# Performance work log

Hardware: AMD Instinct MI355X
Metric: run time of the kernel (lower is better)

## Reference

```python
import jax, jax.numpy as jnp
import numpy as np
from jax import lax

B, C_IN, C_OUT, K, STYLE_DIM, H, W = 8, 512, 512, 3, 512, 64, 64


def setup_inputs() -> dict:
    key = jax.random.key(0)
    k1, k2, k3, k4 = jax.random.split(key, 4)
    return {
        "x": jax.random.normal(k1, (B, C_IN, H, W), dtype=jnp.float32),
        "style": jax.random.normal(k2, (B, STYLE_DIM), dtype=jnp.float32),
        "w": jax.random.normal(k3, (1, C_OUT, C_IN, K, K), dtype=jnp.float32),
        "affine_w": jax.random.normal(k4, (C_IN, STYLE_DIM), dtype=jnp.float32),
        "affine_b": jnp.ones((C_IN,), dtype=jnp.float32),  # bias_init=1
    }


def _per_sample_conv(xi, wi):
    # xi: [C_in, H, W], wi: [C_out, C_in, K, K]; 'same' padding, stride 1
    p = K // 2
    out = lax.conv_general_dilated(
        xi[None], wi, window_strides=(1, 1), padding=[(p, p), (p, p)],
        dimension_numbers=("NCHW", "OIHW", "NCHW"))
    return out[0]


def reference(x, style, w, affine_w, affine_b):
    # Affine (FullyConnected_Layer, linear act, lr_multiplier=1)
    weight_gain_fc = 1.0 / np.sqrt(STYLE_DIM)
    s = style @ (affine_w * weight_gain_fc).T + affine_b  # [B, C_in]

    # Modulate
    weight_gain = 1.0 / np.sqrt(C_IN * K * K)
    weight = w * weight_gain * s[:, None, :, None, None]  # [B, C_out, C_in, K, K]

    # Demodulate
    decoefs = lax.rsqrt(jnp.sum(weight * weight, axis=(2, 3, 4)) + 1e-8)  # [B, C_out]
    weight = weight * decoefs[:, :, None, None, None]

    # Per-sample conv (equivalent to groups=B grouped conv2d)
    out = jax.vmap(_per_sample_conv)(x, weight)  # [B, C_out, H, W]
    return out
```

## Files before the change

kernel.cpp:

```cpp
#include <hip/hip_runtime.h>
#include <hip/hip_bf16.h>


#define CDIM 512
#define HW 64
#define CK 32
#define NCHUNK 16

typedef __attribute__((ext_vector_type(8))) short short8;
typedef __attribute__((ext_vector_type(4))) float float4v;

__device__ __forceinline__ short f2bf(float f) {
    unsigned u = __float_as_uint(f);
    unsigned r = (u + 0x7FFFu + ((u >> 16) & 1u)) >> 16;
    return (short)r;
}

__device__ __forceinline__ void async_ld16(const short* g, short* l) {
    __builtin_amdgcn_global_load_lds(
        (const __attribute__((address_space(1))) void*)g,
        (__attribute__((address_space(3))) void*)l, 16, 0, 0);
}

__device__ __forceinline__ void hard_sync() {
    asm volatile("s_waitcnt vmcnt(0) lgkmcnt(0)" ::: "memory");
    __builtin_amdgcn_sched_barrier(0);
    __builtin_amdgcn_s_barrier();
    __builtin_amdgcn_sched_barrier(0);
}


__global__ void k_affine(const float* __restrict__ style, const float* __restrict__ aw,
                         const float* __restrict__ ab, float* __restrict__ s) {
    int b = blockIdx.x;
    int ci = blockIdx.y * 256 + threadIdx.x;
    const float* st = style + b * CDIM;
    const float* w = aw + ci * CDIM;
    float acc = 0.f;
    for (int k = 0; k < CDIM; ++k) acc += st[k] * w[k];
    s[b * CDIM + ci] = acc * 0.04419417382415922f + ab[ci];
}

__global__ void k_ws2(const float* __restrict__ w, float* __restrict__ ws2) {
    int i = blockIdx.x * 256 + threadIdx.x;
    const float* p = w + i * 9;
    float a = 0.f;
#pragma unroll
    for (int t = 0; t < 9; ++t) a += p[t] * p[t];
    ws2[i] = a;
}

__global__ void k_oscale(const float* __restrict__ s, const float* __restrict__ ws2,
                         float* __restrict__ osc) {
    __shared__ float s2[CDIM];
    int b = blockIdx.x;
    int co = blockIdx.y * 256 + threadIdx.x;
    for (int i = threadIdx.x; i < CDIM; i += 256) {
        float v = s[b * CDIM + i];
        s2[i] = v * v;
    }
    __syncthreads();
    const float* r = ws2 + co * CDIM;
    float acc = 0.f;
    for (int k = 0; k < CDIM; ++k) acc += s2[k] * r[k];
    const float wg = 0.014731391274719739f;
    const float wg2 = 2.170138888888889e-4f;
    osc[b * CDIM + co] = wg * rsqrtf(wg2 * acc + 1e-8f);
}

__global__ void k_wconv(const float* __restrict__ w, short* __restrict__ wgt) {
    int idx = blockIdx.x * 256 + threadIdx.x;
    int j = idx & 7;
    int slotg = idx >> 3;
    int region = slotg / 4608;
    int a16 = slotg - region * 4608;
    int tm = a16 >> 6;
    int t = tm >> 3;
    int mf = tm & 7;
    int sl = a16 & 63;
    int l4 = sl >> 4;
    int l15 = sl & 15;
    int ct = region & 3;
    int c = region >> 2;
    int co = ct * 128 + mf * 16 + l15;
    int ci = c * 32 + l4 * 8 + j;
    wgt[idx] = f2bf(w[(co * CDIM + ci) * 9 + t]);
}

__global__ void k_xs(const float* __restrict__ x, const float* __restrict__ s,
                     short* __restrict__ xs) {
    const int bx = blockIdx.x;
    const int grow = bx & 63;
    const int t = bx >> 6;
    const int c = t & 15;
    const int b = t >> 4;
    const int q = threadIdx.x >> 6;
    const int lane = threadIdx.x & 63;
    const int cig = q ^ (((lane + 1) >> 1) & 3);
    const int ci0 = c * 32 + cig * 8;
    const float* xb = x + ((b * CDIM + ci0) * HW + grow) * HW + lane;
    const float* sb = s + b * CDIM + ci0;
    short8 pk;
#pragma unroll
    for (int j = 0; j < 8; ++j)
        pk[j] = f2bf(xb[j * (HW * HW)] * sb[j]);
    *(short8*)&xs[bx * 2048 + lane * 32 + q * 8] = pk;
}

__global__ __launch_bounds__(512, 1) void conv_main2(
    const short* __restrict__ xs, const short* __restrict__ zs,
    const short* __restrict__ wgt, const float* __restrict__ osc,
    float* __restrict__ out) {

    __shared__ __align__(16) short w_lds[9 * 8 * 64 * 8];
    __shared__ __align__(16) short x_lds[2][10 * 66 * CK];

    const int tid = threadIdx.x;
    const int lane = tid & 63;
    const int wid = tid >> 6;
    const int l15 = lane & 15;
    const int l4 = lane >> 4;

    const int bx = blockIdx.x;
    const int xcd = bx & 7;
    const int t7 = bx >> 3;
    const int ct = t7 & 3;
    const int ghi = t7 >> 2;
    const int b = xcd;
    const int r0 = ghi * 8;

    for (int i = tid; i < 640; i += 512) {
        int bufi = i >= 320;
        int v = i - bufi * 320;
        int row = v >> 5;
        int w16 = v & 31;
        int colh = (w16 >= 16) ? 65 : 0;
        int q16 = w16 & 15;
        ((unsigned*)x_lds[bufi])[(row * 66 + colh) * 16 + q16] = 0u;
    }

    auto stage_w = [&](int c) {
        const short* src = wgt + (c * 4 + ct) * 36864;
#pragma unroll
        for (int k = 0; k < 9; ++k) {
            int off = (k * 512 + wid * 64) * 8;
            async_ld16(src + off + lane * 8, w_lds + off);
        }
    };

    auto stage_x = [&](int c, int buf) {
        const short* xsb = xs + ((b * 16 + c) << 17);
#pragma unroll
        for (int k = 0; k < 5; ++k) {
            int slot = wid * 5 + k;
            int row = slot >> 2;
            int part = slot & 3;
            int grow = r0 - 1 + row;
            const short* src = (grow >= 0 && grow < HW)
                ? xsb + grow * 2048 + part * 512
                : zs + part * 512;
            short* dst = &x_lds[buf][(row * 66 + 1) * CK] + part * 512;
            async_ld16(src + lane * 8, dst + lane * 8);
        }
    };

    float4v acc[8][4] = {};

    auto compute = [&](int buf) {
        const short* xb = x_lds[buf];
#pragma unroll
        for (int t = 0; t < 9; ++t) {
            int dh = t / 3 - 1;
            int dw = t % 3 - 1;
            int lrow = wid + dh + 1;
            short8 bfr[4];
#pragma unroll
            for (int nf = 0; nf < 4; ++nf) {
                int lcol = 1 + nf * 16 + l15 + dw;
                int xq = l4 ^ ((lcol >> 1) & 3);
                bfr[nf] = *(const short8*)&xb[(lrow * 66 + lcol) * CK + xq * 8];
            }
#pragma unroll
            for (int mf = 0; mf < 8; ++mf) {
                short8 af = *(const short8*)&w_lds[((t * 8 + mf) * 64 + lane) * 8];
#pragma unroll
                for (int nf = 0; nf < 4; ++nf)
                    acc[mf][nf] = __builtin_amdgcn_mfma_f32_16x16x32_bf16(
                        af, bfr[nf], acc[mf][nf], 0, 0, 0);
            }
        }
    };

    stage_w(0);
    stage_x(0, 0);
    stage_x(1, 1);
    __builtin_amdgcn_sched_barrier(0);
    asm volatile("s_waitcnt vmcnt(5) lgkmcnt(0)" ::: "memory");
    __builtin_amdgcn_sched_barrier(0);
    __builtin_amdgcn_s_barrier();
    __builtin_amdgcn_sched_barrier(0);

    int cur = 0;
#pragma unroll 1
    for (int c = 0; c < NCHUNK; ++c) {
        __builtin_amdgcn_s_setprio(1);
        compute(cur);
        __builtin_amdgcn_s_setprio(0);

        __builtin_amdgcn_sched_barrier(0);
        asm volatile("s_waitcnt lgkmcnt(0)" ::: "memory");
        __builtin_amdgcn_s_barrier();
        __builtin_amdgcn_sched_barrier(0);

        const int cc1 = (c + 1 < NCHUNK) ? c + 1 : NCHUNK - 1;
        const int cc2 = (c + 2 < NCHUNK) ? c + 2 : NCHUNK - 1;
        stage_w(cc1);
        stage_x(cc2, cur);
        __builtin_amdgcn_sched_barrier(0);

        asm volatile("s_waitcnt vmcnt(5)" ::: "memory");
        __builtin_amdgcn_sched_barrier(0);
        __builtin_amdgcn_s_barrier();
        __builtin_amdgcn_sched_barrier(0);
        cur ^= 1;
    }

    const int row_out = r0 + wid;
#pragma unroll
    for (int mf = 0; mf < 8; ++mf) {
        float4v ov = *(const float4v*)&osc[b * CDIM + ct * 128 + mf * 16 + l4 * 4];
#pragma unroll
        for (int j = 0; j < 4; ++j) {
            int co = ct * 128 + mf * 16 + l4 * 4 + j;
            float* po = out + ((b * CDIM + co) * HW + row_out) * HW;
#pragma unroll
            for (int nf = 0; nf < 4; ++nf)
                po[nf * 16 + l15] = acc[mf][nf][j] * ov[j];
        }
    }
}

__global__ __launch_bounds__(512, 1) void conv_main_fb(
    const float* __restrict__ x, const float* __restrict__ s,
    const short* __restrict__ wgt, const float* __restrict__ osc,
    float* __restrict__ out) {

    __shared__ __align__(16) short w_lds[9 * 8 * 64 * 8];
    __shared__ __align__(16) short x_lds[2][10 * 66 * CK];

    const int tid = threadIdx.x;
    const int lane = tid & 63;
    const int wid = tid >> 6;
    const int l15 = lane & 15;
    const int l4 = lane >> 4;

    const int bx = blockIdx.x;
    const int xcd = bx & 7;
    const int t7 = bx >> 3;
    const int ct = t7 & 3;
    const int ghi = t7 >> 2;
    const int b = xcd;
    const int r0 = ghi * 8;

    const int cig = tid & 3;
    const int col = (tid >> 2) & 63;
    const int rowhalf = tid >> 8;

    for (int i = tid; i < 640; i += 512) {
        int bufi = i >= 320;
        int v = i - bufi * 320;
        int row = v >> 5;
        int w16 = v & 31;
        int colh = (w16 >= 16) ? 65 : 0;
        int q16 = w16 & 15;
        ((unsigned*)x_lds[bufi])[(row * 66 + colh) * 16 + q16] = 0u;
    }

    float rx[40];
    float4v sva, svb;

    auto stage_w = [&](int c) {
        const short* src = wgt + (c * 4 + ct) * 36864;
#pragma unroll
        for (int k = 0; k < 9; ++k) {
            int off = (k * 512 + wid * 64) * 8;
            async_ld16(src + off + lane * 8, w_lds + off);
        }
    };

    auto stage_x_load = [&](int c) {
        const float4v* sp = (const float4v*)&s[b * CDIM + c * 32 + cig * 8];
        sva = sp[0]; svb = sp[1];
#pragma unroll
        for (int i = 0; i < 5; ++i) {
            int row = 2 * i + rowhalf;
            int grow = r0 - 1 + row;
            bool ok = (grow >= 0) && (grow < HW);
            const float* base = x + ((b * CDIM + c * 32 + cig * 8) * HW + (ok ? grow : 0)) * HW + col;
#pragma unroll
            for (int j = 0; j < 8; ++j) {
                float v = base[j * (HW * HW)];
                rx[i * 8 + j] = ok ? v : 0.0f;
            }
        }
    };

    auto stage_x_write = [&](int buf) {
        int lcol = col + 1;
        int q = cig ^ ((lcol >> 1) & 3);
#pragma unroll
        for (int i = 0; i < 5; ++i) {
            int row = 2 * i + rowhalf;
            short8 pk;
#pragma unroll
            for (int j = 0; j < 8; ++j) {
                float sj = (j < 4) ? sva[j] : svb[j - 4];
                pk[j] = f2bf(rx[i * 8 + j] * sj);
            }
            *(short8*)&x_lds[buf][(row * 66 + lcol) * CK + q * 8] = pk;
        }
    };

    float4v acc[8][4] = {};

    auto compute = [&](int buf) {
        const short* xb = x_lds[buf];
#pragma unroll
        for (int t = 0; t < 9; ++t) {
            int dh = t / 3 - 1;
            int dw = t % 3 - 1;
            int lrow = wid + dh + 1;
            short8 bfr[4];
#pragma unroll
            for (int nf = 0; nf < 4; ++nf) {
                int lcol = 1 + nf * 16 + l15 + dw;
                int xq = l4 ^ ((lcol >> 1) & 3);
                bfr[nf] = *(const short8*)&xb[(lrow * 66 + lcol) * CK + xq * 8];
            }
#pragma unroll
            for (int mf = 0; mf < 8; ++mf) {
                short8 af = *(const short8*)&w_lds[((t * 8 + mf) * 64 + lane) * 8];
#pragma unroll
                for (int nf = 0; nf < 4; ++nf)
                    acc[mf][nf] = __builtin_amdgcn_mfma_f32_16x16x32_bf16(
                        af, bfr[nf], acc[mf][nf], 0, 0, 0);
            }
        }
    };

    stage_w(0);
    stage_x_load(0);
    stage_x_write(0);
    hard_sync();

    int cur = 0;
#pragma unroll 1
    for (int c = 0; c < NCHUNK; ++c) {
        if (c + 1 < NCHUNK) stage_x_load(c + 1);
        compute(cur);
        if (c + 1 < NCHUNK) {
            hard_sync();
            stage_w(c + 1);
            stage_x_write(cur ^ 1);
            hard_sync();
            cur ^= 1;
        }
    }

    const int row_out = r0 + wid;
#pragma unroll
    for (int mf = 0; mf < 8; ++mf) {
        float4v ov = *(const float4v*)&osc[b * CDIM + ct * 128 + mf * 16 + l4 * 4];
#pragma unroll
        for (int j = 0; j < 4; ++j) {
            int co = ct * 128 + mf * 16 + l4 * 4 + j;
            float* po = out + ((b * CDIM + co) * HW + row_out) * HW;
#pragma unroll
            for (int nf = 0; nf < 4; ++nf)
                po[nf * 16 + l15] = acc[mf][nf][j] * ov[j];
        }
    }
}


extern "C" void kernel_launch(void* const* d_in, const int* in_sizes, int n_in,
                              void* d_out, int out_size, void* d_ws, size_t ws_size,
                              hipStream_t stream) {
    const float* x     = (const float*)d_in[0];
    const float* style = (const float*)d_in[1];
    const float* w     = (const float*)d_in[2];
    const float* aw    = (const float*)d_in[3];
    const float* ab    = (const float*)d_in[4];
    float* out = (float*)d_out;

    char* wsb = (char*)d_ws;
    float* s_buf = (float*)(wsb);
    float* ws2   = (float*)(wsb + 16384);
    float* osc   = (float*)(wsb + 1064960);
    short* wgt   = (short*)(wsb + 1081344);
    short* zs    = (short*)(wsb + 5799936);
    short* xs    = (short*)(wsb + 5804032);
    const size_t need = 5804032ull + 33554432ull;

    k_affine<<<dim3(8, 2), 256, 0, stream>>>(style, aw, ab, s_buf);
    k_ws2<<<1024, 256, 0, stream>>>(w, ws2);
    k_wconv<<<9216, 256, 0, stream>>>(w, wgt);
    k_oscale<<<dim3(8, 2), 256, 0, stream>>>(s_buf, ws2, osc);

    if (ws_size >= need) {
        hipMemsetAsync(zs, 0, 4096, stream);
        k_xs<<<8192, 256, 0, stream>>>(x, s_buf, xs);
        conv_main2<<<256, 512, 0, stream>>>(xs, zs, wgt, osc, out);
    } else {
        conv_main_fb<<<256, 512, 0, stream>>>(x, s_buf, wgt, osc, out);
    }
}
```

Before: 185.6 us.

## Double conv block to 16 waves splitting output channels; warp-reduce affine and demod kernels

The main conv kernel now runs 1024 threads per block, with each pair of waves sharing an output row and splitting the 8 output-channel fragments 4/4. This halves per-wave accumulators and raises wave count to hide LDS and MFMA latency. Staging loads are redistributed over more threads, with wait counts adjusted to match. The affine and demodulation prep kernels switch from one thread per serial 512-long dot product to one wave per dot product, using vector loads and a shuffle reduction, so they launch far more blocks. The cost is duplicated B-fragment LDS reads across the wave pairs and heavier barrier synchronisation among more waves.

```diff
diff --git a/kernel.cpp b/kernel.cpp
--- a/kernel.cpp
+++ b/kernel.cpp
@@ -32,13 +32,20 @@
 
 __global__ void k_affine(const float* __restrict__ style, const float* __restrict__ aw,
                          const float* __restrict__ ab, float* __restrict__ s) {
-    int b = blockIdx.x;
-    int ci = blockIdx.y * 256 + threadIdx.x;
-    const float* st = style + b * CDIM;
-    const float* w = aw + ci * CDIM;
+    int gid = blockIdx.x * 4 + (threadIdx.x >> 6);
+    int lane = threadIdx.x & 63;
+    int b = gid >> 9, ci = gid & 511;
+    const float4v* st = (const float4v*)(style + b * CDIM);
+    const float4v* wp = (const float4v*)(aw + ci * CDIM);
     float acc = 0.f;
-    for (int k = 0; k < CDIM; ++k) acc += st[k] * w[k];
-    s[b * CDIM + ci] = acc * 0.04419417382415922f + ab[ci];
+#pragma unroll
+    for (int k = 0; k < 2; ++k) {
+        float4v a = st[lane * 2 + k], w = wp[lane * 2 + k];
+        acc += a[0] * w[0] + a[1] * w[1] + a[2] * w[2] + a[3] * w[3];
+    }
+#pragma unroll
+    for (int off = 32; off; off >>= 1) acc += __shfl_down(acc, off);
+    if (lane == 0) s[gid] = acc * 0.04419417382415922f + ab[ci];
 }
 
 __global__ void k_ws2(const float* __restrict__ w, float* __restrict__ ws2) {
@@ -52,20 +59,23 @@
 
 __global__ void k_oscale(const float* __restrict__ s, const float* __restrict__ ws2,
                          float* __restrict__ osc) {
-    __shared__ float s2[CDIM];
-    int b = blockIdx.x;
-    int co = blockIdx.y * 256 + threadIdx.x;
-    for (int i = threadIdx.x; i < CDIM; i += 256) {
-        float v = s[b * CDIM + i];
-        s2[i] = v * v;
-    }
-    __syncthreads();
-    const float* r = ws2 + co * CDIM;
+    int gid = blockIdx.x * 4 + (threadIdx.x >> 6);
+    int lane = threadIdx.x & 63;
+    int b = gid >> 9, co = gid & 511;
+    const float4v* sp = (const float4v*)(s + b * CDIM);
+    const float4v* rp = (const float4v*)(ws2 + co * CDIM);
     float acc = 0.f;
-    for (int k = 0; k < CDIM; ++k) acc += s2[k] * r[k];
+#pragma unroll
+    for (int k = 0; k < 2; ++k) {
+        float4v a = sp[lane * 2 + k], r = rp[lane * 2 + k];
+        acc += a[0] * a[0] * r[0] + a[1] * a[1] * r[1]
+             + a[2] * a[2] * r[2] + a[3] * a[3] * r[3];
+    }
+#pragma unroll
+    for (int off = 32; off; off >>= 1) acc += __shfl_down(acc, off);
     const float wg = 0.014731391274719739f;
     const float wg2 = 2.170138888888889e-4f;
-    osc[b * CDIM + co] = wg * rsqrtf(wg2 * acc + 1e-8f);
+    if (lane == 0) osc[gid] = wg * rsqrtf(wg2 * acc + 1e-8f);
 }
 
 __global__ void k_wconv(const float* __restrict__ w, short* __restrict__ wgt) {
@@ -107,7 +117,7 @@
     *(short8*)&xs[bx * 2048 + lane * 32 + q * 8] = pk;
 }
 
-__global__ __launch_bounds__(512, 1) void conv_main2(
+__global__ __launch_bounds__(1024, 1) void conv_main2(
     const short* __restrict__ xs, const short* __restrict__ zs,
     const short* __restrict__ wgt, const float* __restrict__ osc,
     float* __restrict__ out) {
@@ -118,6 +128,8 @@
     const int tid = threadIdx.x;
     const int lane = tid & 63;
     const int wid = tid >> 6;
+    const int wr = wid >> 1;
+    const int wm = wid & 1;
     const int l15 = lane & 15;
     const int l4 = lane >> 4;
 
@@ -129,9 +141,9 @@
     const int b = xcd;
     const int r0 = ghi * 8;
 
-    for (int i = tid; i < 640; i += 512) {
-        int bufi = i >= 320;
-        int v = i - bufi * 320;
+    if (tid < 640) {
+        int bufi = tid >= 320;
+        int v = tid - bufi * 320;
         int row = v >> 5;
         int w16 = v & 31;
         int colh = (w16 >= 16) ? 65 : 0;
@@ -142,19 +154,21 @@
     auto stage_w = [&](int c) {
         const short* src = wgt + (c * 4 + ct) * 36864;
 #pragma unroll
-        for (int k = 0; k < 9; ++k) {
-            int off = (k * 512 + wid * 64) * 8;
-            async_ld16(src + off + lane * 8, w_lds + off);
+        for (int k = 0; k < 5; ++k) {
+            int u = tid + 1024 * k;
+            if (u >= 4608) u -= 4608;
+            async_ld16(src + u * 8, w_lds + u * 8);
         }
     };
 
     auto stage_x = [&](int c, int buf) {
         const short* xsb = xs + ((b * 16 + c) << 17);
 #pragma unroll
-        for (int k = 0; k < 5; ++k) {
-            int slot = wid * 5 + k;
-            int row = slot >> 2;
-            int part = slot & 3;
+        for (int k = 0; k < 3; ++k) {
+            int u = wid + 16 * k;
+            if (u >= 40) u -= 40;
+            int row = u >> 2;
+            int part = u & 3;
             int grow = r0 - 1 + row;
             const short* src = (grow >= 0 && grow < HW)
                 ? xsb + grow * 2048 + part * 512
@@ -164,7 +178,7 @@
         }
     };
 
-    float4v acc[8][4] = {};
+    float4v acc[4][4] = {};
 
     auto compute = [&](int buf) {
         const short* xb = x_lds[buf];
@@ -172,7 +186,7 @@
         for (int t = 0; t < 9; ++t) {
             int dh = t / 3 - 1;
             int dw = t % 3 - 1;
-            int lrow = wid + dh + 1;
+            int lrow = wr + dh + 1;
             short8 bfr[4];
 #pragma unroll
             for (int nf = 0; nf < 4; ++nf) {
@@ -181,8 +195,8 @@
                 bfr[nf] = *(const short8*)&xb[(lrow * 66 + lcol) * CK + xq * 8];
             }
 #pragma unroll
-            for (int mf = 0; mf < 8; ++mf) {
-                short8 af = *(const short8*)&w_lds[((t * 8 + mf) * 64 + lane) * 8];
+            for (int mf = 0; mf < 4; ++mf) {
+                short8 af = *(const short8*)&w_lds[((t * 8 + wm * 4 + mf) * 64 + lane) * 8];
 #pragma unroll
                 for (int nf = 0; nf < 4; ++nf)
                     acc[mf][nf] = __builtin_amdgcn_mfma_f32_16x16x32_bf16(
@@ -195,7 +209,7 @@
     stage_x(0, 0);
     stage_x(1, 1);
     __builtin_amdgcn_sched_barrier(0);
-    asm volatile("s_waitcnt vmcnt(5) lgkmcnt(0)" ::: "memory");
+    asm volatile("s_waitcnt vmcnt(3) lgkmcnt(0)" ::: "memory");
     __builtin_amdgcn_sched_barrier(0);
     __builtin_amdgcn_s_barrier();
     __builtin_amdgcn_sched_barrier(0);
@@ -218,20 +232,22 @@
         stage_x(cc2, cur);
         __builtin_amdgcn_sched_barrier(0);
 
-        asm volatile("s_waitcnt vmcnt(5)" ::: "memory");
+        asm volatile("s_waitcnt vmcnt(3)" ::: "memory");
         __builtin_amdgcn_sched_barrier(0);
         __builtin_amdgcn_s_barrier();
         __builtin_amdgcn_sched_barrier(0);
         cur ^= 1;
     }
 
-    const int row_out = r0 + wid;
-#pragma unroll
-    for (int mf = 0; mf < 8; ++mf) {
-        float4v ov = *(const float4v*)&osc[b * CDIM + ct * 128 + mf * 16 + l4 * 4];
+    asm volatile("s_waitcnt vmcnt(0)" ::: "memory");
+
+    const int row_out = r0 + wr;
+#pragma unroll
+    for (int mf = 0; mf < 4; ++mf) {
+        float4v ov = *(const float4v*)&osc[b * CDIM + ct * 128 + (wm * 4 + mf) * 16 + l4 * 4];
 #pragma unroll
         for (int j = 0; j < 4; ++j) {
-            int co = ct * 128 + mf * 16 + l4 * 4 + j;
+            int co = ct * 128 + (wm * 4 + mf) * 16 + l4 * 4 + j;
             float* po = out + ((b * CDIM + co) * HW + row_out) * HW;
 #pragma unroll
             for (int nf = 0; nf < 4; ++nf)
@@ -402,15 +418,15 @@
     short* xs    = (short*)(wsb + 5804032);
     const size_t need = 5804032ull + 33554432ull;
 
-    k_affine<<<dim3(8, 2), 256, 0, stream>>>(style, aw, ab, s_buf);
+    k_affine<<<1024, 256, 0, stream>>>(style, aw, ab, s_buf);
     k_ws2<<<1024, 256, 0, stream>>>(w, ws2);
     k_wconv<<<9216, 256, 0, stream>>>(w, wgt);
-    k_oscale<<<dim3(8, 2), 256, 0, stream>>>(s_buf, ws2, osc);
+    k_oscale<<<1024, 256, 0, stream>>>(s_buf, ws2, osc);
 
     if (ws_size >= need) {
         hipMemsetAsync(zs, 0, 4096, stream);
         k_xs<<<8192, 256, 0, stream>>>(x, s_buf, xs);
-        conv_main2<<<256, 512, 0, stream>>>(xs, zs, wgt, osc, out);
+        conv_main2<<<256, 1024, 0, stream>>>(xs, zs, wgt, osc, out);
     } else {
         conv_main_fb<<<256, 512, 0, stream>>>(x, s_buf, wgt, osc, out);
     }
```

After: 180.3 us. -2.9%, faster.
